# Kernel optimization log

Measured on AMD Instinct MI355X. Metric: run time of the kernel, lower is better.

## Reference

```python
import jax, jax.numpy as jnp
import numpy as np

EMB = 384
HID = 256
HEADS = 4
HD = HID // HEADS  # 64
LAYERS = 2
M_DOCS = 32
TOTAL = 4096  # 1 query + 32 docs + 4063 sentences
LN_EPS = 1e-5


def _layernorm(x, scale, bias):
    mu = jnp.mean(x, axis=-1, keepdims=True)
    var = jnp.mean(jnp.square(x - mu), axis=-1, keepdims=True)
    return (x - mu) * jax.lax.rsqrt(var + LN_EPS) * scale + bias


def setup_inputs() -> dict:
    key = jax.random.key(0)
    ks = jax.random.split(key, 12)
    g = 0.05  # small init scale (stand-in for xavier)
    return {
        "node_embeddings": jax.random.normal(ks[0], (TOTAL, EMB), jnp.float32),
        "adj": jax.random.randint(ks[1], (TOTAL, TOTAL), 0, 2, jnp.int32),
        "num_docs": M_DOCS,
        "proj_w": jax.random.normal(ks[2], (HID, EMB), jnp.float32) * g,
        "proj_b": jnp.zeros((HID,), jnp.float32),
        "ln_scale": jnp.ones((LAYERS, HID), jnp.float32),
        "ln_bias": jnp.zeros((LAYERS, HID), jnp.float32),
        "gat_W": jax.random.normal(ks[3], (LAYERS, HEADS, HD, HID), jnp.float32) * g,
        "gat_a": jax.random.normal(ks[4], (LAYERS, HEADS, 2 * HD), jnp.float32) * g,
        "fusion_w": jax.random.normal(ks[5], (HID, 2 * HID + 2), jnp.float32) * g,
        "fusion_b": jnp.zeros((HID,), jnp.float32),
        "out_w": jax.random.normal(ks[6], (HID,), jnp.float32) * g,
        "out_b": jnp.float32(0.5),
    }


def reference(node_embeddings, adj, num_docs, proj_w, proj_b, ln_scale, ln_bias,
              gat_W, gat_a, fusion_w, fusion_b, out_w, out_b):
    T = node_embeddings.shape[0]
    M = num_docs
    N = T - 1 - M  # number of sentences
    # input projection + relu (dropout = identity in eval)
    h = jax.nn.relu(node_embeddings @ proj_w.T + proj_b)  # (T, HID)
    # query-guided sentence re-weighting
    q = h[0:1]                     # (1, HID)
    s = h[1 + M:]                  # (N, HID)
    qn = q / (jnp.linalg.norm(q, axis=1, keepdims=True) + 1e-8)
    sn = s / (jnp.linalg.norm(s, axis=1, keepdims=True) + 1e-8)
    cos = (qn @ sn.T).reshape(-1, 1)          # (N,1)
    s = s + 0.8 * q * cos
    h = jnp.concatenate([h[:1 + M], s], axis=0)
    mask = (adj == 0)[None]                   # (1,T,T)
    for i in range(LAYERS):
        res = h
        x = _layernorm(h, ln_scale[i], ln_bias[i])
        Wh = jnp.einsum('nd,hkd->hnk', x, gat_W[i])                # (H,T,HD)
        # concat-attention a.[Wh_i ; Wh_j] == a_src.Wh_i + a_dst.Wh_j
        src = jnp.einsum('hnk,hk->hn', Wh, gat_a[i, :, :HD])       # (H,T)
        dst = jnp.einsum('hnk,hk->hn', Wh, gat_a[i, :, HD:])       # (H,T)
        e = jax.nn.leaky_relu(src[:, :, None] + dst[:, None, :], 0.2)  # (H,T,T)
        e = jnp.where(mask, -jnp.inf, e)
        attn = jax.nn.softmax(e, axis=-1)                          # softmax over j
        hn = jnp.einsum('hij,hjk->hik', attn, Wh)                  # (H,T,HD)
        hcat = jnp.transpose(hn, (1, 0, 2)).reshape(T, HEADS * HD)
        h = 0.5 * jax.nn.relu(hcat) + 0.5 * res
    qh = h[0:1]
    sh = h[1 + M:]
    scores = (qh @ sh.T) / (HID ** 0.5)       # (1,N)
    aw = jax.nn.softmax(scores, axis=-1)
    awT = aw.T                                # (N,1)
    qw = qh * (awT + 0.5)                     # (N,HID)
    qnf = qh / (jnp.linalg.norm(qh, axis=1, keepdims=True) + 1e-8)
    snf = sh / (jnp.linalg.norm(sh, axis=1, keepdims=True) + 1e-8)
    cosf = (qnf @ snf.T).reshape(-1, 1)       # (N,1)
    feat = jnp.concatenate([sh, qw, cosf, awT], axis=1)  # (N, 2*HID+2)
    g = jax.nn.relu(feat @ fusion_w.T + fusion_b)
    out = g @ out_w + out_b                   # (N,)
    return out + 0.5 * cosf[:, 0]
```

## Files before the change

### kernel.cpp

```cpp
#include <hip/hip_runtime.h>
#include <hip/hip_bf16.h>
#include <stdint.h>

#define TOTAL 4096
#define EMB 384
#define MD 32
#define NDOCS (TOTAL - 1 - MD)
#define LN_EPS 1e-5f

typedef __hip_bfloat16 bf16;
typedef unsigned short ushort_t;
typedef __attribute__((ext_vector_type(8))) short short8;
typedef __attribute__((ext_vector_type(4))) float f32x4;

__device__ __forceinline__ float ldf(const void* p, int i, int isbf) {
    return isbf ? __bfloat162float(((const bf16*)p)[i]) : ((const float*)p)[i];
}

__device__ __forceinline__ ushort_t f2bf(float x) {
    return (ushort_t)((__float_as_uint(x) + 0x8000u) >> 16);
}

__global__ void k_detect(const uint16_t* p, int* flag) {
    __shared__ int red[4];
    int t = threadIdx.x;
    int cnt = 0;
    for (int k = t; k < 4096; k += 256) {
        uint16_t w = p[2 * k];
        int e = (w >> 7) & 0xFF;
        if (e >= 100 && e <= 140) cnt++;
    }
    for (int o = 32; o > 0; o >>= 1) cnt += __shfl_down(cnt, o);
    if ((t & 63) == 0) red[t >> 6] = cnt;
    __syncthreads();
    if (t == 0) flag[0] = (red[0] + red[1] + red[2] + red[3] > 2048) ? 1 : 0;
}

__global__ void k_transpose(const void* proj_w, const void* gat_W, const void* fusion_w,
                            float* projT, float* gatT, float* fwT, const int* flagp) {
    int isbf = flagp[0];
    int idx = blockIdx.x * 256 + threadIdx.x;
    if (idx < EMB * 256) {
        int d = idx >> 8, c = idx & 255;
        projT[idx] = ldf(proj_w, c * EMB + d, isbf);
    } else if (idx < EMB * 256 + 2 * 256 * 256) {
        int r = idx - EMB * 256;
        int l = r >> 16; int rem = r & 65535;
        int d = rem >> 8, c = rem & 255;
        gatT[r] = ldf(gat_W, l * 65536 + c * 256 + d, isbf);
    } else if (idx < EMB * 256 + 2 * 256 * 256 + 514 * 256) {
        int r = idx - (EMB * 256 + 2 * 256 * 256);
        int j = r >> 8, c = r & 255;
        fwT[r] = ldf(fusion_w, c * 514 + j, isbf);
    }
}

__global__ void k_adjmask(const int* adj, unsigned long long* maskb) {
    int i = blockIdx.x;
    int t = threadIdx.x;
    int w = t >> 6, l = t & 63;
    for (int c = w; c < 64; c += 4) {
        int a = adj[(size_t)i * TOTAL + c * 64 + l];
        unsigned long long m = __ballot(a != 0);
        if (l == 0) maskb[i * 64 + c] = m;
    }
}

#define PR 8
__global__ void k_proj(const void* emb, const void* proj_b, const float* projT, float* h,
                       const int* flagp) {
    __shared__ float xs[PR][EMB];
    int isbf = flagp[0];
    int i0 = blockIdx.x * PR, t = threadIdx.x;
    for (int idx = t; idx < PR * EMB; idx += 256) {
        int r = idx / EMB, d = idx % EMB;
        xs[r][d] = ldf(emb, (i0 + r) * EMB + d, isbf);
    }
    __syncthreads();
    float acc[PR];
    float bias = ldf(proj_b, t, isbf);
#pragma unroll
    for (int r = 0; r < PR; r++) acc[r] = bias;
    for (int d = 0; d < EMB; d++) {
        float wv = projT[d * 256 + t];
#pragma unroll
        for (int r = 0; r < PR; r++) acc[r] = fmaf(xs[r][d], wv, acc[r]);
    }
#pragma unroll
    for (int r = 0; r < PR; r++) h[(size_t)(i0 + r) * 256 + t] = fmaxf(acc[r], 0.f);
}

__global__ __launch_bounds__(256) void k_cosupdate(float* h) {
    int t = threadIdx.x, W = t >> 6, lane = t & 63;
    float4* h4 = (float4*)h;
    float4 q4 = h4[lane];
    float a = q4.x * q4.x + q4.y * q4.y + q4.z * q4.z + q4.w * q4.w;
    for (int o = 32; o > 0; o >>= 1) a += __shfl_xor(a, o);
    float qn = sqrtf(a) + 1e-8f;
    int gw = blockIdx.x * 4 + W;
    for (int n = gw; n < NDOCS; n += 1024) {
        size_t ro = (size_t)(1 + MD + n) * 64;
        float4 s4 = h4[ro + lane];
        float b = s4.x * s4.x + s4.y * s4.y + s4.z * s4.z + s4.w * s4.w;
        float c = q4.x * s4.x + q4.y * s4.y + q4.z * s4.z + q4.w * s4.w;
        for (int o = 32; o > 0; o >>= 1) { b += __shfl_xor(b, o); c += __shfl_xor(c, o); }
        float k = 0.8f * (c / (qn * (sqrtf(b) + 1e-8f)));
        s4.x += k * q4.x; s4.y += k * q4.y; s4.z += k * q4.z; s4.w += k * q4.w;
        h4[ro + lane] = s4;
    }
}

#define LR 4
__global__ void k_ln_wh(const float* h, const float* gatT, const void* ln_scale,
                        const void* ln_bias, const void* gat_a,
                        ushort_t* whswz, float* srcb, float* dstb, float2* dpre,
                        int layer, const int* flagp) {
    __shared__ float xs[LR][256];
    __shared__ float red[2][LR][4];
    int isbf = flagp[0];
    int i0 = blockIdx.x * LR, t = threadIdx.x;
    int w = t >> 6, l = t & 63;
    float scale = ldf(ln_scale, layer * 256 + t, isbf);
    float bias = ldf(ln_bias, layer * 256 + t, isbf);
    float hv[LR];
#pragma unroll
    for (int r = 0; r < LR; r++) hv[r] = h[(size_t)(i0 + r) * 256 + t];
#pragma unroll
    for (int r = 0; r < LR; r++) {
        float a = hv[r], b = hv[r] * hv[r];
        for (int o = 32; o > 0; o >>= 1) { a += __shfl_down(a, o); b += __shfl_down(b, o); }
        if (l == 0) { red[0][r][w] = a; red[1][r][w] = b; }
    }
    __syncthreads();
#pragma unroll
    for (int r = 0; r < LR; r++) {
        float mu = (red[0][r][0] + red[0][r][1] + red[0][r][2] + red[0][r][3]) * (1.f / 256.f);
        float var = (red[1][r][0] + red[1][r][1] + red[1][r][2] + red[1][r][3]) * (1.f / 256.f) - mu * mu;
        float x = (hv[r] - mu) * rsqrtf(var + LN_EPS) * scale + bias;
        xs[r][t] = x;
    }
    __syncthreads();
    const float* gT = gatT + layer * 65536;
    float acc[LR] = {0.f, 0.f, 0.f, 0.f};
    for (int d = 0; d < 256; d++) {
        float wv = gT[d * 256 + t];
#pragma unroll
        for (int r = 0; r < LR; r++) acc[r] = fmaf(xs[r][d], wv, acc[r]);
    }
    float av1 = ldf(gat_a, layer * 512 + w * 128 + l, isbf);
    float av2 = ldf(gat_a, layer * 512 + w * 128 + 64 + l, isbf);
    const float LOG2E = 1.44269504f;
#pragma unroll
    for (int r = 0; r < LR; r++) {
        int i = i0 + r;
        int off = (i >> 6) * 16384 + (t >> 6) * 4096 + ((i >> 3) & 7) * 512 +
                  ((t >> 4) & 3) * 128 + (t & 15) * 8 + (i & 7);
        whswz[off] = f2bf(acc[r]);
        float sv = acc[r] * av1, dv = acc[r] * av2;
        for (int o = 32; o > 0; o >>= 1) { sv += __shfl_down(sv, o); dv += __shfl_down(dv, o); }
        if (l == 0) {
            srcb[w * 4096 + i] = sv;
            dstb[w * 4096 + i] = dv;
            dpre[w * 4096 + i] = make_float2(dv * LOG2E, 0.2f * dv * LOG2E);
        }
    }
}

__global__ void k_dmax(const float* dstb, float* dmax) {
    __shared__ float red[4];
    int h = blockIdx.x, t = threadIdx.x;
    float m = -__builtin_inff();
    for (int j = t; j < 4096; j += 256) m = fmaxf(m, dstb[h * 4096 + j]);
    for (int o = 32; o > 0; o >>= 1) m = fmaxf(m, __shfl_down(m, o));
    if ((t & 63) == 0) red[t >> 6] = m;
    __syncthreads();
    if (t == 0) dmax[h] = fmaxf(fmaxf(red[0], red[1]), fmaxf(red[2], red[3]));
}

#define TI 32
#define JS 4
__global__ __launch_bounds__(512) void k_pv(const ushort_t* whswz, const float* srcb,
                                            const float* dmax, const float2* dpre,
                                            const unsigned long long* maskb,
                                            float* hnp, float* lpart) {
    __shared__ unsigned long long mbs[TI][17];
    __shared__ float2 dpres[4][1024];
    __shared__ float srcs[4][TI], rces[4][TI];
    f32x4* accsh = (f32x4*)dpres;
    int t = threadIdx.x;
    int W = t >> 6, lane = t & 63;
    int h = W & 3, kq = W >> 2;
    int quad = lane >> 4, c16 = lane & 15;
    int i0 = blockIdx.x * TI;
    int jbase = blockIdx.y * 1024;
    for (int idx = t; idx < TI * 16; idx += 512) {
        int r = idx >> 4, wd = idx & 15;
        mbs[r][wd] = maskb[(size_t)(i0 + r) * 64 + (jbase >> 6) + wd];
    }
    for (int idx = t; idx < 4096; idx += 512) {
        int hh = idx >> 10, jl = idx & 1023;
        dpres[hh][jl] = dpre[hh * 4096 + jbase + jl];
    }
    if (t < 128) {
        int h2 = t >> 5, r = t & 31;
        float sv = srcb[h2 * 4096 + i0 + r];
        srcs[h2][r] = sv;
        float sd = sv + dmax[h2];
        rces[h2][r] = -fmaxf(sd, 0.2f * sd);
    }
    __syncthreads();
    const float LOG2E = 1.44269504f;
    float s1[2], s2[2], psum[2] = {0.f, 0.f};
#pragma unroll
    for (int rt = 0; rt < 2; rt++) {
        float src = srcs[h][rt * 16 + c16], rce = rces[h][rt * 16 + c16];
        s1[rt] = (src + rce) * LOG2E;
        s2[rt] = (0.2f * src + rce) * LOG2E;
    }
    f32x4 acc[2][4];
#pragma unroll
    for (int rt = 0; rt < 2; rt++)
#pragma unroll
        for (int ct = 0; ct < 4; ct++) acc[rt][ct] = (f32x4){0.f, 0.f, 0.f, 0.f};
    const uint4* g4 = (const uint4*)whswz;
    size_t b0 = (size_t)(jbase >> 6) * 2048 + h * 512 + (kq * 4 + quad) * 64 + c16;
    uint4 bn[4];
#pragma unroll
    for (int ct = 0; ct < 4; ct++) bn[ct] = g4[b0 + ct * 16];
    for (int step = 0; step < 16; step++) {
        uint4 bc[4];
#pragma unroll
        for (int ct = 0; ct < 4; ct++) bc[ct] = bn[ct];
        if (step < 15) {
            size_t bs = b0 + (size_t)(step + 1) * 2048;
#pragma unroll
            for (int ct = 0; ct < 4; ct++) bn[ct] = g4[bs + ct * 16];
        }
        int jl0 = step * 64 + kq * 32 + quad * 8;
        unsigned int mby[2];
#pragma unroll
        for (int rt = 0; rt < 2; rt++)
            mby[rt] = (unsigned int)(mbs[rt * 16 + c16][step] >> (kq * 32 + quad * 8)) & 0xFFu;
        const float4* dp4 = (const float4*)&dpres[h][jl0];
        float4 dv[4];
#pragma unroll
        for (int q = 0; q < 4; q++) dv[q] = dp4[q];
        short8 af[2];
#pragma unroll
        for (int rt = 0; rt < 2; rt++) {
#pragma unroll
            for (int q = 0; q < 4; q++) {
                float4 d = dv[q];
                float pa = exp2f(fmaxf(s1[rt] + d.x, s2[rt] + d.y));
                float pb = exp2f(fmaxf(s1[rt] + d.z, s2[rt] + d.w));
                pa = ((mby[rt] >> (2 * q)) & 1u) ? pa : 0.f;
                pb = ((mby[rt] >> (2 * q + 1)) & 1u) ? pb : 0.f;
                psum[rt] += pa + pb;
                af[rt][2 * q] = (short)f2bf(pa);
                af[rt][2 * q + 1] = (short)f2bf(pb);
            }
        }
#pragma unroll
        for (int ct = 0; ct < 4; ct++) {
            short8 bf = __builtin_bit_cast(short8, bc[ct]);
            acc[0][ct] = __builtin_amdgcn_mfma_f32_16x16x32_bf16(af[0], bf, acc[0][ct], 0, 0, 0);
            acc[1][ct] = __builtin_amdgcn_mfma_f32_16x16x32_bf16(af[1], bf, acc[1][ct], 0, 0, 0);
        }
    }
#pragma unroll
    for (int rt = 0; rt < 2; rt++) {
        float ps = psum[rt];
        ps += __shfl_xor(ps, 16);
        ps += __shfl_xor(ps, 32);
        if (quad == 0)
            lpart[((blockIdx.y * 4 + h) * 2 + kq) * 4096 + i0 + rt * 16 + c16] = ps;
    }
    __syncthreads();
    if (kq == 1) {
#pragma unroll
        for (int rt = 0; rt < 2; rt++)
#pragma unroll
            for (int ct = 0; ct < 4; ct++)
                accsh[((h * 2 + rt) * 4 + ct) * 64 + lane] = acc[rt][ct];
    }
    __syncthreads();
    if (kq == 0) {
        float* out = hnp + (size_t)blockIdx.y * (TOTAL * 256);
#pragma unroll
        for (int rt = 0; rt < 2; rt++)
#pragma unroll
            for (int ct = 0; ct < 4; ct++) {
                f32x4 o = acc[rt][ct] + accsh[((h * 2 + rt) * 4 + ct) * 64 + lane];
#pragma unroll
                for (int rr = 0; rr < 4; rr++) {
                    int row = i0 + rt * 16 + quad * 4 + rr;
                    out[(size_t)row * 256 + h * 64 + ct * 16 + c16] = o[rr];
                }
            }
    }
}

__global__ void k_epilogue(const float* hnp, const float* lpart, float* h) {
    int idx = blockIdx.x * 256 + threadIdx.x;
    int row = idx >> 6, hh_ = (idx >> 4) & 3;
    float l = 0.f;
#pragma unroll
    for (int js = 0; js < 4; js++)
#pragma unroll
        for (int kq = 0; kq < 2; kq++)
            l += lpart[((js * 4 + hh_) * 2 + kq) * 4096 + row];
    float inv = 1.f / l;
    const float4* p0 = (const float4*)hnp;
    const float4* p1 = (const float4*)(hnp + (size_t)TOTAL * 256);
    const float4* p2 = (const float4*)(hnp + (size_t)2 * TOTAL * 256);
    const float4* p3 = (const float4*)(hnp + (size_t)3 * TOTAL * 256);
    float4* h4 = (float4*)h;
    float4 a = p0[idx], b = p1[idx], c = p2[idx], d = p3[idx], hh = h4[idx];
    hh.x = 0.5f * fmaxf((a.x + b.x + c.x + d.x) * inv, 0.f) + 0.5f * hh.x;
    hh.y = 0.5f * fmaxf((a.y + b.y + c.y + d.y) * inv, 0.f) + 0.5f * hh.y;
    hh.z = 0.5f * fmaxf((a.z + b.z + c.z + d.z) * inv, 0.f) + 0.5f * hh.z;
    hh.w = 0.5f * fmaxf((a.w + b.w + c.w + d.w) * inv, 0.f) + 0.5f * hh.w;
    h4[idx] = hh;
}

__global__ __launch_bounds__(256) void k_scores(const float* h, float* scoresv, float* cosv) {
    int t = threadIdx.x, W = t >> 6, lane = t & 63;
    const float4* h4 = (const float4*)h;
    float4 q4 = h4[lane];
    float a = q4.x * q4.x + q4.y * q4.y + q4.z * q4.z + q4.w * q4.w;
    for (int o = 32; o > 0; o >>= 1) a += __shfl_xor(a, o);
    float qn = sqrtf(a) + 1e-8f;
    int gw = blockIdx.x * 4 + W;
    for (int n = gw; n < NDOCS; n += 1024) {
        size_t ro = (size_t)(1 + MD + n) * 64;
        float4 s4 = h4[ro + lane];
        float b = s4.x * s4.x + s4.y * s4.y + s4.z * s4.z + s4.w * s4.w;
        float c = q4.x * s4.x + q4.y * s4.y + q4.z * s4.z + q4.w * s4.w;
        for (int o = 32; o > 0; o >>= 1) { b += __shfl_xor(b, o); c += __shfl_xor(c, o); }
        if (lane == 0) {
            scoresv[n] = c * (1.f / 16.f);
            cosv[n] = c / (qn * (sqrtf(b) + 1e-8f));
        }
    }
}

__global__ void k_softmax(const float* scoresv, float* awv) {
    __shared__ float red[4];
    int t = threadIdx.x;
    float m = -__builtin_inff();
    for (int n = t; n < NDOCS; n += 256) m = fmaxf(m, scoresv[n]);
    for (int o = 32; o > 0; o >>= 1) m = fmaxf(m, __shfl_down(m, o));
    if ((t & 63) == 0) red[t >> 6] = m;
    __syncthreads();
    m = fmaxf(fmaxf(red[0], red[1]), fmaxf(red[2], red[3]));
    __syncthreads();
    float s = 0.f;
    for (int n = t; n < NDOCS; n += 256) s += __expf(scoresv[n] - m);
    for (int o = 32; o > 0; o >>= 1) s += __shfl_down(s, o);
    if ((t & 63) == 0) red[t >> 6] = s;
    __syncthreads();
    s = red[0] + red[1] + red[2] + red[3];
    float inv = 1.f / s;
    for (int n = t; n < NDOCS; n += 256) awv[n] = __expf(scoresv[n] - m) * inv;
}

#define TN 8
__global__ __launch_bounds__(256) void k_fusion(const float* h, const float* awv,
                                                const float* cosv, const float* fwT,
                                                const void* fusion_b, const void* out_w,
                                                const void* out_bp, void* outv,
                                                const int* flagp) {
    __shared__ float feats[TN][516];
    __shared__ float qhs[256];
    __shared__ float red[TN][4];
    int isbf = flagp[0];
    int t = threadIdx.x;
    int n0 = blockIdx.x * TN;
    qhs[t] = h[t];
    __syncthreads();
    for (int idx = t; idx < TN * 514; idx += 256) {
        int r = idx / 514, j = idx % 514;
        int n = n0 + r;
        float v = 0.f;
        if (n < NDOCS) {
            if (j < 256) v = h[(size_t)(1 + MD + n) * 256 + j];
            else if (j < 512) v = qhs[j - 256] * (awv[n] + 0.5f);
            else if (j == 512) v = cosv[n];
            else v = awv[n];
        }
        feats[r][j] = v;
    }
    __syncthreads();
    float acc[TN];
    float bk = ldf(fusion_b, t, isbf);
#pragma unroll
    for (int r = 0; r < TN; r++) acc[r] = bk;
    for (int j0 = 0; j0 < 512; j0 += 8) {
        float wv[8];
#pragma unroll
        for (int u = 0; u < 8; u++) wv[u] = fwT[(j0 + u) * 256 + t];
#pragma unroll
        for (int u = 0; u < 8; u++)
#pragma unroll
            for (int r = 0; r < TN; r++) acc[r] = fmaf(feats[r][j0 + u], wv[u], acc[r]);
    }
#pragma unroll
    for (int j = 512; j < 514; j++) {
        float wv = fwT[j * 256 + t];
#pragma unroll
        for (int r = 0; r < TN; r++) acc[r] = fmaf(feats[r][j], wv, acc[r]);
    }
    float ow = ldf(out_w, t, isbf);
    float outb = ldf(out_bp, 0, isbf);
#pragma unroll
    for (int r = 0; r < TN; r++) {
        float o = fmaxf(acc[r], 0.f) * ow;
        for (int off = 32; off > 0; off >>= 1) o += __shfl_down(o, off);
        if ((t & 63) == 0) red[r][t >> 6] = o;
    }
    __syncthreads();
    if (t < TN) {
        int n = n0 + t;
        if (n < NDOCS) {
            float o = red[t][0] + red[t][1] + red[t][2] + red[t][3] + outb + 0.5f * cosv[n];
            if (isbf) ((bf16*)outv)[n] = __float2bfloat16(o);
            else      ((float*)outv)[n] = o;
        }
    }
}

extern "C" void kernel_launch(void* const* d_in, const int* in_sizes, int n_in,
                              void* d_out, int out_size, void* d_ws, size_t ws_size,
                              hipStream_t stream) {
    const void* emb      = d_in[0];
    const int*  adj      = (const int*)d_in[1];
    const void* proj_w   = d_in[3];
    const void* proj_b   = d_in[4];
    const void* ln_scale = d_in[5];
    const void* ln_bias  = d_in[6];
    const void* gat_W    = d_in[7];
    const void* gat_a    = d_in[8];
    const void* fusion_w = d_in[9];
    const void* fusion_b = d_in[10];
    const void* out_w    = d_in[11];
    const void* out_b    = d_in[12];

    unsigned long long* maskb = (unsigned long long*)d_ws;
    int* flag = (int*)((char*)d_ws + (size_t)4096 * 64 * 8);
    float* f = (float*)((char*)d_ws + (size_t)4096 * 64 * 8 + 256);
    float* h       = f; f += 4096 * 256;
    float* srcb    = f; f += 4 * 4096;
    float* dstb    = f; f += 4 * 4096;
    float2* dpre   = (float2*)f; f += 2 * 4 * 4096;
    float* dmax    = f; f += 64;
    float* projT   = f; f += EMB * 256;
    float* gatT    = f; f += 2 * 256 * 256;
    float* fwT     = f; f += 514 * 256;
    float* scoresv = f; f += 4096;
    float* cosv    = f; f += 4096;
    float* awv     = f; f += 4096;
    float* lpart   = f; f += 4 * 4 * 2 * 4096;
    ushort_t* whswz = (ushort_t*)f; f += 4096 * 256 / 2;
    float* hnp     = f; f += (size_t)JS * 4096 * 256;

    k_detect<<<dim3(1), dim3(256), 0, stream>>>((const uint16_t*)emb, flag);
    k_transpose<<<dim3(1410), dim3(256), 0, stream>>>(proj_w, gat_W, fusion_w, projT, gatT, fwT, flag);
    k_adjmask<<<dim3(4096), dim3(256), 0, stream>>>(adj, maskb);
    k_proj<<<dim3(TOTAL / PR), dim3(256), 0, stream>>>(emb, proj_b, projT, h, flag);
    k_cosupdate<<<dim3(256), dim3(256), 0, stream>>>(h);
    for (int layer = 0; layer < 2; layer++) {
        k_ln_wh<<<dim3(TOTAL / LR), dim3(256), 0, stream>>>(h, gatT, ln_scale, ln_bias, gat_a,
                                                            whswz, srcb, dstb, dpre, layer, flag);
        k_dmax<<<dim3(4), dim3(256), 0, stream>>>(dstb, dmax);
        k_pv<<<dim3(TOTAL / TI, JS), dim3(512), 0, stream>>>(whswz, srcb, dmax, dpre,
                                                             maskb, hnp, lpart);
        k_epilogue<<<dim3(1024), dim3(256), 0, stream>>>(hnp, lpart, h);
    }
    k_scores<<<dim3(256), dim3(256), 0, stream>>>(h, scoresv, cosv);
    k_softmax<<<dim3(1), dim3(256), 0, stream>>>(scoresv, awv);
    k_fusion<<<dim3((NDOCS + TN - 1) / TN), dim3(256), 0, stream>>>(h, awv, cosv, fwT,
                                                                    fusion_b, out_w, out_b,
                                                                    (void*)d_out, flag);
}
```

Measured before the change: 357.1 us.

## Compute softmax row sums via MFMA, split dpre arrays, vectorize LDS reads

In the attention kernel, the softmax denominator is no longer accumulated with scalar adds. It is now computed by an extra MFMA against a ones vector, and the per-pair mask is applied with a bitmask lookup on packed bf16. The dst precompute is split into two float arrays so packed f32x2 math can be used, and the lpart partials drop the kq dimension. The projection, LN-Wh and fusion GEMV loops read LDS as float4, and the final softmax runs with 1024 threads. The aim is to cut VALU work in the hot attention loop, at the cost of extra MFMA issue and denominators summed from bf16-rounded probabilities.

Result: faster. 342.6 us (-4.1%).

```diff
diff --git a/kernel.cpp b/kernel.cpp
--- a/kernel.cpp
+++ b/kernel.cpp
@@ -12,6 +12,7 @@
 typedef unsigned short ushort_t;
 typedef __attribute__((ext_vector_type(8))) short short8;
 typedef __attribute__((ext_vector_type(4))) float f32x4;
+typedef __attribute__((ext_vector_type(2))) float f32x2;
 
 __device__ __forceinline__ float ldf(const void* p, int i, int isbf) {
     return isbf ? __bfloat162float(((const bf16*)p)[i]) : ((const float*)p)[i];
@@ -81,10 +82,19 @@
     float bias = ldf(proj_b, t, isbf);
 #pragma unroll
     for (int r = 0; r < PR; r++) acc[r] = bias;
-    for (int d = 0; d < EMB; d++) {
-        float wv = projT[d * 256 + t];
-#pragma unroll
-        for (int r = 0; r < PR; r++) acc[r] = fmaf(xs[r][d], wv, acc[r]);
+    for (int d0 = 0; d0 < EMB; d0 += 4) {
+        float w0 = projT[d0 * 256 + t];
+        float w1 = projT[(d0 + 1) * 256 + t];
+        float w2 = projT[(d0 + 2) * 256 + t];
+        float w3 = projT[(d0 + 3) * 256 + t];
+#pragma unroll
+        for (int r = 0; r < PR; r++) {
+            float4 x = *(const float4*)&xs[r][d0];
+            acc[r] = fmaf(x.x, w0, acc[r]);
+            acc[r] = fmaf(x.y, w1, acc[r]);
+            acc[r] = fmaf(x.z, w2, acc[r]);
+            acc[r] = fmaf(x.w, w3, acc[r]);
+        }
     }
 #pragma unroll
     for (int r = 0; r < PR; r++) h[(size_t)(i0 + r) * 256 + t] = fmaxf(acc[r], 0.f);
@@ -113,7 +123,7 @@
 #define LR 4
 __global__ void k_ln_wh(const float* h, const float* gatT, const void* ln_scale,
                         const void* ln_bias, const void* gat_a,
-                        ushort_t* whswz, float* srcb, float* dstb, float2* dpre,
+                        ushort_t* whswz, float* srcb, float* dstb, float* d1g, float* d2g,
                         int layer, const int* flagp) {
     __shared__ float xs[LR][256];
     __shared__ float red[2][LR][4];
@@ -142,10 +152,19 @@
     __syncthreads();
     const float* gT = gatT + layer * 65536;
     float acc[LR] = {0.f, 0.f, 0.f, 0.f};
-    for (int d = 0; d < 256; d++) {
-        float wv = gT[d * 256 + t];
-#pragma unroll
-        for (int r = 0; r < LR; r++) acc[r] = fmaf(xs[r][d], wv, acc[r]);
+    for (int d0 = 0; d0 < 256; d0 += 4) {
+        float w0 = gT[d0 * 256 + t];
+        float w1 = gT[(d0 + 1) * 256 + t];
+        float w2 = gT[(d0 + 2) * 256 + t];
+        float w3 = gT[(d0 + 3) * 256 + t];
+#pragma unroll
+        for (int r = 0; r < LR; r++) {
+            float4 x = *(const float4*)&xs[r][d0];
+            acc[r] = fmaf(x.x, w0, acc[r]);
+            acc[r] = fmaf(x.y, w1, acc[r]);
+            acc[r] = fmaf(x.z, w2, acc[r]);
+            acc[r] = fmaf(x.w, w3, acc[r]);
+        }
     }
     float av1 = ldf(gat_a, layer * 512 + w * 128 + l, isbf);
     float av2 = ldf(gat_a, layer * 512 + w * 128 + 64 + l, isbf);
@@ -161,7 +180,8 @@
         if (l == 0) {
             srcb[w * 4096 + i] = sv;
             dstb[w * 4096 + i] = dv;
-            dpre[w * 4096 + i] = make_float2(dv * LOG2E, 0.2f * dv * LOG2E);
+            d1g[w * 4096 + i] = dv * LOG2E;
+            d2g[w * 4096 + i] = 0.2f * dv * LOG2E;
         }
     }
 }
@@ -180,26 +200,32 @@
 #define TI 32
 #define JS 4
 __global__ __launch_bounds__(512) void k_pv(const ushort_t* whswz, const float* srcb,
-                                            const float* dmax, const float2* dpre,
+                                            const float* dmax, const float* d1g,
+                                            const float* d2g,
                                             const unsigned long long* maskb,
                                             float* hnp, float* lpart) {
     __shared__ unsigned long long mbs[TI][17];
-    __shared__ float2 dpres[4][1024];
+    __shared__ float d1s[4][1024];
+    __shared__ float d2s[4][1024];
     __shared__ float srcs[4][TI], rces[4][TI];
-    f32x4* accsh = (f32x4*)dpres;
+    __shared__ unsigned int mlut[4];
+    __shared__ __align__(16) float lsh[4][2][4][4];
+    f32x4* accsh = (f32x4*)d1s;
     int t = threadIdx.x;
     int W = t >> 6, lane = t & 63;
     int h = W & 3, kq = W >> 2;
     int quad = lane >> 4, c16 = lane & 15;
     int i0 = blockIdx.x * TI;
     int jbase = blockIdx.y * 1024;
+    if (t < 4) mlut[t] = (t & 1 ? 0x0000FFFFu : 0u) | (t & 2 ? 0xFFFF0000u : 0u);
     for (int idx = t; idx < TI * 16; idx += 512) {
         int r = idx >> 4, wd = idx & 15;
         mbs[r][wd] = maskb[(size_t)(i0 + r) * 64 + (jbase >> 6) + wd];
     }
-    for (int idx = t; idx < 4096; idx += 512) {
-        int hh = idx >> 10, jl = idx & 1023;
-        dpres[hh][jl] = dpre[hh * 4096 + jbase + jl];
+    for (int idx = t; idx < 1024; idx += 512) {
+        int hh = idx >> 8, j4 = idx & 255;
+        ((float4*)d1s)[idx] = ((const float4*)(d1g + hh * 4096 + jbase))[j4];
+        ((float4*)d2s)[idx] = ((const float4*)(d2g + hh * 4096 + jbase))[j4];
     }
     if (t < 128) {
         int h2 = t >> 5, r = t & 31;
@@ -210,7 +236,7 @@
     }
     __syncthreads();
     const float LOG2E = 1.44269504f;
-    float s1[2], s2[2], psum[2] = {0.f, 0.f};
+    float s1[2], s2[2];
 #pragma unroll
     for (int rt = 0; rt < 2; rt++) {
         float src = srcs[h][rt * 16 + c16], rce = rces[h][rt * 16 + c16];
@@ -218,10 +244,15 @@
         s2[rt] = (0.2f * src + rce) * LOG2E;
     }
     f32x4 acc[2][4];
+    f32x4 accl[2] = {(f32x4){0.f, 0.f, 0.f, 0.f}, (f32x4){0.f, 0.f, 0.f, 0.f}};
 #pragma unroll
     for (int rt = 0; rt < 2; rt++)
 #pragma unroll
         for (int ct = 0; ct < 4; ct++) acc[rt][ct] = (f32x4){0.f, 0.f, 0.f, 0.f};
+    uint4 onesu;
+    unsigned os = (c16 == 0) ? 0x3F803F80u : 0u;
+    onesu.x = os; onesu.y = os; onesu.z = os; onesu.w = os;
+    short8 bfones = __builtin_bit_cast(short8, onesu);
     const uint4* g4 = (const uint4*)whswz;
     size_t b0 = (size_t)(jbase >> 6) * 2048 + h * 512 + (kq * 4 + quad) * 64 + c16;
     uint4 bn[4];
@@ -241,53 +272,52 @@
 #pragma unroll
         for (int rt = 0; rt < 2; rt++)
             mby[rt] = (unsigned int)(mbs[rt * 16 + c16][step] >> (kq * 32 + quad * 8)) & 0xFFu;
-        const float4* dp4 = (const float4*)&dpres[h][jl0];
-        float4 dv[4];
-#pragma unroll
-        for (int q = 0; q < 4; q++) dv[q] = dp4[q];
-        short8 af[2];
+        const f32x2* p1 = (const f32x2*)&d1s[h][jl0];
+        const f32x2* p2 = (const f32x2*)&d2s[h][jl0];
+        f32x2 d1v[4] = {p1[0], p1[1], p1[2], p1[3]};
+        f32x2 d2v[4] = {p2[0], p2[1], p2[2], p2[3]};
+        uint4 afu[2];
 #pragma unroll
         for (int rt = 0; rt < 2; rt++) {
+            unsigned pu[4];
 #pragma unroll
             for (int q = 0; q < 4; q++) {
-                float4 d = dv[q];
-                float pa = exp2f(fmaxf(s1[rt] + d.x, s2[rt] + d.y));
-                float pb = exp2f(fmaxf(s1[rt] + d.z, s2[rt] + d.w));
-                pa = ((mby[rt] >> (2 * q)) & 1u) ? pa : 0.f;
-                pb = ((mby[rt] >> (2 * q + 1)) & 1u) ? pb : 0.f;
-                psum[rt] += pa + pb;
-                af[rt][2 * q] = (short)f2bf(pa);
-                af[rt][2 * q + 1] = (short)f2bf(pb);
+                f32x2 t1 = d1v[q] + s1[rt];
+                f32x2 t2 = d2v[q] + s2[rt];
+                f32x2 m = __builtin_elementwise_max(t1, t2);
+                float ea = exp2f(m.x), eb = exp2f(m.y);
+                unsigned v = ((__float_as_uint(ea) + 0x8000u) >> 16) |
+                             ((__float_as_uint(eb) + 0x8000u) & 0xFFFF0000u);
+                pu[q] = v & mlut[(mby[rt] >> (2 * q)) & 3u];
             }
-        }
+            afu[rt].x = pu[0]; afu[rt].y = pu[1]; afu[rt].z = pu[2]; afu[rt].w = pu[3];
+        }
+        short8 af0 = __builtin_bit_cast(short8, afu[0]);
+        short8 af1 = __builtin_bit_cast(short8, afu[1]);
 #pragma unroll
         for (int ct = 0; ct < 4; ct++) {
             short8 bf = __builtin_bit_cast(short8, bc[ct]);
-            acc[0][ct] = __builtin_amdgcn_mfma_f32_16x16x32_bf16(af[0], bf, acc[0][ct], 0, 0, 0);
-            acc[1][ct] = __builtin_amdgcn_mfma_f32_16x16x32_bf16(af[1], bf, acc[1][ct], 0, 0, 0);
-        }
-    }
-#pragma unroll
-    for (int rt = 0; rt < 2; rt++) {
-        float ps = psum[rt];
-        ps += __shfl_xor(ps, 16);
-        ps += __shfl_xor(ps, 32);
-        if (quad == 0)
-            lpart[((blockIdx.y * 4 + h) * 2 + kq) * 4096 + i0 + rt * 16 + c16] = ps;
+            acc[0][ct] = __builtin_amdgcn_mfma_f32_16x16x32_bf16(af0, bf, acc[0][ct], 0, 0, 0);
+            acc[1][ct] = __builtin_amdgcn_mfma_f32_16x16x32_bf16(af1, bf, acc[1][ct], 0, 0, 0);
+        }
+        accl[0] = __builtin_amdgcn_mfma_f32_16x16x32_bf16(af0, bfones, accl[0], 0, 0, 0);
+        accl[1] = __builtin_amdgcn_mfma_f32_16x16x32_bf16(af1, bfones, accl[1], 0, 0, 0);
     }
     __syncthreads();
     if (kq == 1) {
 #pragma unroll
-        for (int rt = 0; rt < 2; rt++)
+        for (int rt = 0; rt < 2; rt++) {
 #pragma unroll
             for (int ct = 0; ct < 4; ct++)
                 accsh[((h * 2 + rt) * 4 + ct) * 64 + lane] = acc[rt][ct];
+            if (c16 == 0) *(f32x4*)&lsh[h][rt][quad][0] = accl[rt];
+        }
     }
     __syncthreads();
     if (kq == 0) {
         float* out = hnp + (size_t)blockIdx.y * (TOTAL * 256);
 #pragma unroll
-        for (int rt = 0; rt < 2; rt++)
+        for (int rt = 0; rt < 2; rt++) {
 #pragma unroll
             for (int ct = 0; ct < 4; ct++) {
                 f32x4 o = acc[rt][ct] + accsh[((h * 2 + rt) * 4 + ct) * 64 + lane];
@@ -297,6 +327,13 @@
                     out[(size_t)row * 256 + h * 64 + ct * 16 + c16] = o[rr];
                 }
             }
+            if (c16 == 0) {
+                f32x4 lv = accl[rt] + *(const f32x4*)&lsh[h][rt][quad][0];
+#pragma unroll
+                for (int rr = 0; rr < 4; rr++)
+                    lpart[(size_t)(blockIdx.y * 4 + h) * 4096 + i0 + rt * 16 + quad * 4 + rr] = lv[rr];
+            }
+        }
     }
 }
 
@@ -306,9 +343,7 @@
     float l = 0.f;
 #pragma unroll
     for (int js = 0; js < 4; js++)
-#pragma unroll
-        for (int kq = 0; kq < 2; kq++)
-            l += lpart[((js * 4 + hh_) * 2 + kq) * 4096 + row];
+        l += lpart[(size_t)(js * 4 + hh_) * 4096 + row];
     float inv = 1.f / l;
     const float4* p0 = (const float4*)hnp;
     const float4* p1 = (const float4*)(hnp + (size_t)TOTAL * 256);
@@ -344,24 +379,28 @@
     }
 }
 
-__global__ void k_softmax(const float* scoresv, float* awv) {
-    __shared__ float red[4];
+__global__ __launch_bounds__(1024) void k_softmax(const float* scoresv, float* awv) {
+    __shared__ float red[16];
     int t = threadIdx.x;
     float m = -__builtin_inff();
-    for (int n = t; n < NDOCS; n += 256) m = fmaxf(m, scoresv[n]);
+    for (int n = t; n < NDOCS; n += 1024) m = fmaxf(m, scoresv[n]);
     for (int o = 32; o > 0; o >>= 1) m = fmaxf(m, __shfl_down(m, o));
     if ((t & 63) == 0) red[t >> 6] = m;
     __syncthreads();
-    m = fmaxf(fmaxf(red[0], red[1]), fmaxf(red[2], red[3]));
+    m = red[0];
+#pragma unroll
+    for (int i = 1; i < 16; i++) m = fmaxf(m, red[i]);
     __syncthreads();
     float s = 0.f;
-    for (int n = t; n < NDOCS; n += 256) s += __expf(scoresv[n] - m);
+    for (int n = t; n < NDOCS; n += 1024) s += __expf(scoresv[n] - m);
     for (int o = 32; o > 0; o >>= 1) s += __shfl_down(s, o);
     if ((t & 63) == 0) red[t >> 6] = s;
     __syncthreads();
-    s = red[0] + red[1] + red[2] + red[3];
+    s = 0.f;
+#pragma unroll
+    for (int i = 0; i < 16; i++) s += red[i];
     float inv = 1.f / s;
-    for (int n = t; n < NDOCS; n += 256) awv[n] = __expf(scoresv[n] - m) * inv;
+    for (int n = t; n < NDOCS; n += 1024) awv[n] = __expf(scoresv[n] - m) * inv;
 }
 
 #define TN 8
@@ -370,7 +409,7 @@
                                                 const void* fusion_b, const void* out_w,
                                                 const void* out_bp, void* outv,
                                                 const int* flagp) {
-    __shared__ float feats[TN][516];
+    __shared__ float feats2[514][TN];
     __shared__ float qhs[256];
     __shared__ float red[TN][4];
     int isbf = flagp[0];
@@ -378,8 +417,8 @@
     int n0 = blockIdx.x * TN;
     qhs[t] = h[t];
     __syncthreads();
-    for (int idx = t; idx < TN * 514; idx += 256) {
-        int r = idx / 514, j = idx % 514;
+    for (int idx = t; idx < 514 * TN; idx += 256) {
+        int j = idx >> 3, r = idx & 7;
         int n = n0 + r;
         float v = 0.f;
         if (n < NDOCS) {
@@ -388,7 +427,7 @@
             else if (j == 512) v = cosv[n];
             else v = awv[n];
         }
-        feats[r][j] = v;
+        feats2[j][r] = v;
     }
     __syncthreads();
     float acc[TN];
@@ -400,15 +439,24 @@
 #pragma unroll
         for (int u = 0; u < 8; u++) wv[u] = fwT[(j0 + u) * 256 + t];
 #pragma unroll
-        for (int u = 0; u < 8; u++)
-#pragma unroll
-            for (int r = 0; r < TN; r++) acc[r] = fmaf(feats[r][j0 + u], wv[u], acc[r]);
+        for (int u = 0; u < 8; u++) {
+            float4 a = *(const float4*)&feats2[j0 + u][0];
+            float4 b = *(const float4*)&feats2[j0 + u][4];
+            acc[0] = fmaf(a.x, wv[u], acc[0]);
+            acc[1] = fmaf(a.y, wv[u], acc[1]);
+            acc[2] = fmaf(a.z, wv[u], acc[2]);
+            acc[3] = fmaf(a.w, wv[u], acc[3]);
+            acc[4] = fmaf(b.x, wv[u], acc[4]);
+            acc[5] = fmaf(b.y, wv[u], acc[5]);
+            acc[6] = fmaf(b.z, wv[u], acc[6]);
+            acc[7] = fmaf(b.w, wv[u], acc[7]);
+        }
     }
 #pragma unroll
     for (int j = 512; j < 514; j++) {
         float wv = fwT[j * 256 + t];
 #pragma unroll
-        for (int r = 0; r < TN; r++) acc[r] = fmaf(feats[r][j], wv, acc[r]);
+        for (int r = 0; r < TN; r++) acc[r] = fmaf(feats2[j][r], wv, acc[r]);
     }
     float ow = ldf(out_w, t, isbf);
     float outb = ldf(out_bp, 0, isbf);
@@ -451,7 +499,8 @@
     float* h       = f; f += 4096 * 256;
     float* srcb    = f; f += 4 * 4096;
     float* dstb    = f; f += 4 * 4096;
-    float2* dpre   = (float2*)f; f += 2 * 4 * 4096;
+    float* d1g     = f; f += 4 * 4096;
+    float* d2g     = f; f += 4 * 4096;
     float* dmax    = f; f += 64;
     float* projT   = f; f += EMB * 256;
     float* gatT    = f; f += 2 * 256 * 256;
@@ -459,7 +508,7 @@
     float* scoresv = f; f += 4096;
     float* cosv    = f; f += 4096;
     float* awv     = f; f += 4096;
-    float* lpart   = f; f += 4 * 4 * 2 * 4096;
+    float* lpart   = f; f += 4 * 4 * 4096;
     ushort_t* whswz = (ushort_t*)f; f += 4096 * 256 / 2;
     float* hnp     = f; f += (size_t)JS * 4096 * 256;
 
@@ -470,14 +519,14 @@
     k_cosupdate<<<dim3(256), dim3(256), 0, stream>>>(h);
     for (int layer = 0; layer < 2; layer++) {
         k_ln_wh<<<dim3(TOTAL / LR), dim3(256), 0, stream>>>(h, gatT, ln_scale, ln_bias, gat_a,
-                                                            whswz, srcb, dstb, dpre, layer, flag);
+                                                            whswz, srcb, dstb, d1g, d2g, layer, flag);
         k_dmax<<<dim3(4), dim3(256), 0, stream>>>(dstb, dmax);
-        k_pv<<<dim3(TOTAL / TI, JS), dim3(512), 0, stream>>>(whswz, srcb, dmax, dpre,
+        k_pv<<<dim3(TOTAL / TI, JS), dim3(512), 0, stream>>>(whswz, srcb, dmax, d1g, d2g,
                                                              maskb, hnp, lpart);
         k_epilogue<<<dim3(1024), dim3(256), 0, stream>>>(hnp, lpart, h);
     }
     k_scores<<<dim3(256), dim3(256), 0, stream>>>(h, scoresv, cosv);
-    k_softmax<<<dim3(1), dim3(256), 0, stream>>>(scoresv, awv);
+    k_softmax<<<dim3(1), dim3(1024), 0, stream>>>(scoresv, awv);
     k_fusion<<<dim3((NDOCS + TN - 1) / TN), dim3(256), 0, stream>>>(h, awv, cosv, fwT,
                                                                     fusion_b, out_w, out_b,
                                                                     (void*)d_out, flag);
```
